# Performance work log

Hardware: AMD Instinct MI355X
Metric: run time of the kernel (lower is better)

## Reference

```python
import jax, jax.numpy as jnp
import numpy as np

TEMP = 0.5
LAMDA = 1.0
NUM_SLICE = 64
EPS = 1e-20


def _gaussian_kernel(size=11, sigma=1.5):
    coords = np.arange(size, dtype=np.float64) - (size - 1) / 2.0
    g = np.exp(-(coords ** 2) / (2.0 * sigma ** 2))
    g = g / g.sum()
    return jnp.asarray(g, dtype=jnp.float32)


def _ssim(x, y, data_range=1.0, win_size=11, sigma=1.5):
    # x, y: [B, S, H, W]; treat each slice as an independent 1-channel image.
    B, S, H, W = x.shape
    x4 = x.reshape(B * S, 1, H, W)
    y4 = y.reshape(B * S, 1, H, W)
    g = _gaussian_kernel(win_size, sigma)
    kh = g.reshape(1, 1, win_size, 1)
    kw = g.reshape(1, 1, 1, win_size)
    dn = ('NCHW', 'OIHW', 'NCHW')

    def blur(a):
        a = jax.lax.conv_general_dilated(a, kh, (1, 1), 'VALID', dimension_numbers=dn)
        a = jax.lax.conv_general_dilated(a, kw, (1, 1), 'VALID', dimension_numbers=dn)
        return a

    mu1 = blur(x4)
    mu2 = blur(y4)
    mu1_sq = mu1 * mu1
    mu2_sq = mu2 * mu2
    mu1_mu2 = mu1 * mu2
    sigma1_sq = blur(x4 * x4) - mu1_sq
    sigma2_sq = blur(y4 * y4) - mu2_sq
    sigma12 = blur(x4 * y4) - mu1_mu2
    C1 = (0.01 * data_range) ** 2
    C2 = (0.03 * data_range) ** 2
    ssim_map = ((2.0 * mu1_mu2 + C1) * (2.0 * sigma12 + C2)) / (
        (mu1_sq + mu2_sq + C1) * (sigma1_sq + sigma2_sq + C2))
    return jnp.mean(ssim_map)


def _l1(a, b):
    return jnp.mean(jnp.abs(a - b))


def _cumulative_mips(img_fake, target, gumbel, temp):
    # Growing-window gumbel-softmax MIP, computed in a single O(S) pass.
    # softmax over a prefix window is shift-invariant, so subtract the
    # per-pixel global max over the slice axis for stability, then use cumsums.
    y = img_fake + gumbel
    m = jnp.max(y, axis=1, keepdims=True)
    e = jnp.exp((y - m) / temp)                      # unnormalized softmax weights
    num = jnp.cumsum(e * img_fake, axis=1)
    den = jnp.cumsum(e, axis=1)
    pred_c1 = num / den                              # prefix windows [0:idx+1]
    target_c1 = jax.lax.cummax(target, axis=1)

    ef = jnp.flip(e, axis=1)
    xf = jnp.flip(img_fake, axis=1)
    num2 = jnp.cumsum(ef * xf, axis=1)
    den2 = jnp.cumsum(ef, axis=1)
    pred_c2 = num2 / den2                            # suffix windows [S-1-idx:]
    target_c2 = jax.lax.cummax(jnp.flip(target, axis=1), axis=1)
    return pred_c1, target_c1, pred_c2, target_c2


def _forward(img_fake, target, u_noise):
    gumbel = -jnp.log(-jnp.log(u_noise + EPS) + EPS)
    p1, t1, p2, t2 = _cumulative_mips(img_fake, target, gumbel, TEMP)
    loss_lissim = (_l1(img_fake, target) + 1.0 - _ssim(img_fake, target)) * LAMDA
    loss_mip_c1 = (_l1(p1, t1) + 1.0 - _ssim(p1, t1)) * LAMDA
    loss_mip_c2 = (_l1(p2, t2) + 1.0 - _ssim(p2, t2)) * LAMDA
    return loss_lissim + loss_mip_c1 + loss_mip_c2


def setup_inputs() -> dict:
    key = jax.random.key(0)
    k1, k2, k3 = jax.random.split(key, 3)
    shape = (2, NUM_SLICE, 256, 256)
    img_fake = jax.random.uniform(k1, shape, dtype=jnp.float32)
    target = jax.random.uniform(k2, shape, dtype=jnp.float32)
    u_noise = jax.random.uniform(k3, shape, dtype=jnp.float32)
    return {"img_fake": img_fake, "target": target, "u_noise": u_noise}


def reference(img_fake, target, u_noise):
    return _forward(img_fake, target, u_noise)
```

## Files before the change

### kernel.cpp

```cpp
#include <hip/hip_runtime.h>
#include <cmath>
#include <cstring>

#define NUM_S   64
#define IMG_H   256
#define IMG_W   256
#define HWSZ    (IMG_H*IMG_W)
#define BATCH   2
#define NPIX    (BATCH*HWSZ)
#define NEL     (BATCH*NUM_S*HWSZ)
#define NSLICE  (BATCH*NUM_S)
#define VALID   246
#define EPS_F   1e-20f
#define C1_F    1e-4f
#define C2_F    9e-4f
#define RS      264
#define FS      (16*RS)
#define NSLOT_SCAN 1024
#define NSLOT_ALL  7168
#define PTPAD   1024

typedef __fp16 half8  __attribute__((ext_vector_type(8)));
typedef __fp16 fp16x2 __attribute__((ext_vector_type(2)));
using fragC = __attribute__((ext_vector_type(4))) float;

union H8 { half8 v; short s[8]; int i[4]; };
union PK { fp16x2 v; int i; };
union HS { __fp16 f; short s; };

struct GH { short h[11]; };

__device__ inline fp16x2 pkrtz(float a, float b) {
    return __builtin_amdgcn_cvt_pkrtz(a, b);
}
__device__ inline float frcp(float x)  { return __builtin_amdgcn_rcpf(x); }
__device__ inline float flog2(float x) { return __builtin_amdgcn_logf(x); }
__device__ inline float fexp2(float x) { return __builtin_amdgcn_exp2f(x); }

__device__ inline void block_reduce_slot(float v, float* slot) {
    __shared__ float sm[8];
    __syncthreads();
    #pragma unroll
    for (int off = 32; off; off >>= 1) v += __shfl_down(v, off, 64);
    int lane = threadIdx.x & 63, w = threadIdx.x >> 6;
    if (lane == 0) sm[w] = v;
    __syncthreads();
    if (threadIdx.x == 0) {
        float s = 0.f;
        int nw = blockDim.x >> 6;
        for (int i = 0; i < nw; ++i) s += sm[i];
        *slot = s;
    }
}

__global__ __launch_bounds__(256) void scan_kernel(
    const float* __restrict__ img, const float* __restrict__ tgt,
    const float* __restrict__ un,
    uint2* __restrict__ pt0, uint2* __restrict__ pt1, uint2* __restrict__ pt2,
    float* __restrict__ slots)
{
    const int HW2 = HWSZ / 2;
    int tid = blockIdx.x * 256 + threadIdx.x;
    bool bwd = tid >= (NPIX / 2);
    int p2 = bwd ? tid - NPIX / 2 : tid;
    int b   = p2 >> 15;
    int hw2 = p2 & (HW2 - 1);
    int idx  = b * (NUM_S * HW2) + hw2 + (bwd ? (NUM_S - 1) * HW2 : 0);
    int step = bwd ? -HW2 : HW2;
    const float2* __restrict__ img2 = (const float2*)img;
    const float2* __restrict__ tgt2 = (const float2*)tgt;
    const float2* __restrict__ un2  = (const float2*)un;

    float num[2] = {0.f, 0.f}, den[2] = {0.f, 0.f}, tm[2] = {-INFINITY, -INFINITY};
    float l1x = 0.f, l1p = 0.f;

    float2 xb[4], ub[4], tb[4];
    #pragma unroll
    for (int j = 0; j < 4; ++j) {
        int id = idx + j * step;
        xb[j] = img2[id]; ub[j] = un2[id]; tb[j] = tgt2[id];
    }

    for (int i = 0; i < NUM_S; i += 4) {
        #pragma unroll
        for (int j = 0; j < 4; ++j) {
            float2 x = xb[j], u = ub[j], t = tb[j];
            if (i + j + 4 < NUM_S) {
                int id = idx + 4 * step;
                xb[j] = img2[id]; ub[j] = un2[id]; tb[j] = tgt2[id];
            }
            float xc[2] = {x.x, x.y}, uc[2] = {u.x, u.y}, tc[2] = {t.x, t.y};
            float p[2];
            #pragma unroll
            for (int c = 0; c < 2; ++c) {
                float w = fmaf(flog2(uc[c] + EPS_F), -0.6931471805599453f, EPS_F);
                float r = frcp(w);
                float e = fexp2(xc[c] * 2.8853900817779268f) * (r * r);
                num[c] = fmaf(e, xc[c], num[c]);
                den[c] += e;
                p[c] = num[c] * frcp(den[c]);
                tm[c] = fmaxf(tm[c], tc[c]);
                if (!bwd) l1x += fabsf(xc[c] - tc[c]);
                l1p += fabsf(p[c] - tm[c]);
            }
            PK k0, k1;
            k0.v = pkrtz(p[0], tm[0]); k1.v = pkrtz(p[1], tm[1]);
            uint2 pv = make_uint2((unsigned)k0.i, (unsigned)k1.i);
            if (!bwd) {
                PK a0, a1;
                a0.v = pkrtz(xc[0], tc[0]); a1.v = pkrtz(xc[1], tc[1]);
                pt0[idx] = make_uint2((unsigned)a0.i, (unsigned)a1.i);
                pt1[idx] = pv;
            } else {
                pt2[idx] = pv;
            }
            idx += step;
        }
    }
    block_reduce_slot(bwd ? 0.f : l1x, &slots[blockIdx.x]);
    block_reduce_slot(l1p, &slots[512 + blockIdx.x]);
}

__global__ __launch_bounds__(256) void ssim_kernel(
    const unsigned* __restrict__ pt0, const unsigned* __restrict__ pt1,
    const unsigned* __restrict__ pt2,
    GH gh, float* __restrict__ slots)
{
    __shared__ short Vl[5][FS];
    int pair  = blockIdx.z;
    int base  = blockIdx.y * HWSZ;
    int r0    = blockIdx.x * 16;
    int lane  = threadIdx.x & 63;
    int wid   = threadIdx.x >> 6;
    int q     = lane >> 4;
    int n     = lane & 15;

    H8 band;
    #pragma unroll
    for (int j = 0; j < 8; ++j) {
        int kk = q * 8 + j - n;
        short hv = 0;
        #pragma unroll
        for (int w = 0; w < 11; ++w) hv = (kk == w) ? gh.h[w] : hv;
        band.s[j] = hv;
    }

    for (int d = threadIdx.x; d < 320; d += 256) {
        int f = d >> 6, rm = d & 63, r = rm >> 2, cc = rm & 3;
        ((int*)Vl)[f * 2112 + r * 132 + 128 + cc] = 0;
    }

    const unsigned* __restrict__ pp =
        (pair == 0 ? pt0 : (pair == 1 ? pt1 : pt2)) + base;
    bool clampR = (r0 == 240);
    const fragC zero = {0.f, 0.f, 0.f, 0.f};

    unsigned ld[32];
    {
        int rowbase = r0 + q * 8;
        if (!clampR) {
            const unsigned* pb = pp + rowbase * IMG_W + n;
            #pragma unroll
            for (int it = 0; it < 4; ++it)
                #pragma unroll
                for (int j = 0; j < 8; ++j)
                    ld[it * 8 + j] = pb[j * IMG_W + (wid * 4 + it) * 16];
        } else {
            #pragma unroll
            for (int it = 0; it < 4; ++it)
                #pragma unroll
                for (int j = 0; j < 8; ++j) {
                    int rr = min(rowbase + j, IMG_H - 1);
                    ld[it * 8 + j] = pp[rr * IMG_W + (wid * 4 + it) * 16 + n];
                }
        }
    }
    #pragma unroll
    for (int it = 0; it < 4; ++it) {
        H8 fX, fY, fXX, fYY, fXY;
        #pragma unroll
        for (int j = 0; j < 4; ++j) {
            unsigned a = ld[it * 8 + 2 * j], b2 = ld[it * 8 + 2 * j + 1];
            fX.i[j] = (int)((a & 0xffffu) | (b2 << 16));
            fY.i[j] = (int)((a >> 16) | (b2 & 0xffff0000u));
        }
        fXX.v = fX.v * fX.v;
        fYY.v = fY.v * fY.v;
        fXY.v = fX.v * fY.v;
        fragC v0 = __builtin_amdgcn_mfma_f32_16x16x32_f16(band.v, fX.v,  zero, 0, 0, 0);
        fragC v1 = __builtin_amdgcn_mfma_f32_16x16x32_f16(band.v, fY.v,  zero, 0, 0, 0);
        fragC v2 = __builtin_amdgcn_mfma_f32_16x16x32_f16(band.v, fXX.v, zero, 0, 0, 0);
        fragC v3 = __builtin_amdgcn_mfma_f32_16x16x32_f16(band.v, fYY.v, zero, 0, 0, 0);
        fragC v4 = __builtin_amdgcn_mfma_f32_16x16x32_f16(band.v, fXY.v, zero, 0, 0, 0);
        int col = (wid * 4 + it) * 16 + n;
        #pragma unroll
        for (int reg = 0; reg < 4; ++reg) {
            int ro = (q * 4 + reg) * RS + col;
            HS cv;
            cv.f = (__fp16)v0[reg]; Vl[0][ro] = cv.s;
            cv.f = (__fp16)v1[reg]; Vl[1][ro] = cv.s;
            cv.f = (__fp16)v2[reg]; Vl[2][ro] = cv.s;
            cv.f = (__fp16)v3[reg]; Vl[3][ro] = cv.s;
            cv.f = (__fp16)v4[reg]; Vl[4][ro] = cv.s;
        }
    }
    __syncthreads();

    float lsum = 0.f;
    for (int it = 0; it < 4; ++it) {
        int c0 = (wid * 4 + it) * 16;
        int so = n * RS + c0 + q * 8;
        so = min(so, FS - 8);
        H8 a0, a1, a2, a3, a4;
        *(int4*)a0.i = *(const int4*)&Vl[0][so];
        *(int4*)a1.i = *(const int4*)&Vl[1][so];
        *(int4*)a2.i = *(const int4*)&Vl[2][so];
        *(int4*)a3.i = *(const int4*)&Vl[3][so];
        *(int4*)a4.i = *(const int4*)&Vl[4][so];
        fragC o0 = __builtin_amdgcn_mfma_f32_16x16x32_f16(a0.v, band.v, zero, 0, 0, 0);
        fragC o1 = __builtin_amdgcn_mfma_f32_16x16x32_f16(a1.v, band.v, zero, 0, 0, 0);
        fragC o2 = __builtin_amdgcn_mfma_f32_16x16x32_f16(a2.v, band.v, zero, 0, 0, 0);
        fragC o3 = __builtin_amdgcn_mfma_f32_16x16x32_f16(a3.v, band.v, zero, 0, 0, 0);
        fragC o4 = __builtin_amdgcn_mfma_f32_16x16x32_f16(a4.v, band.v, zero, 0, 0, 0);
        #pragma unroll
        for (int reg = 0; reg < 4; ++reg) {
            int r = r0 + q * 4 + reg;
            int c = c0 + n;
            if (r < VALID && c < VALID) {
                float m1 = o0[reg], m2 = o1[reg];
                float s11 = o2[reg] - m1 * m1;
                float s22 = o3[reg] - m2 * m2;
                float s12 = o4[reg] - m1 * m2;
                float nv = (2.f * m1 * m2 + C1_F) * (2.f * s12 + C2_F);
                float dv = (m1 * m1 + m2 * m2 + C1_F) * (s11 + s22 + C2_F);
                lsum += nv * frcp(dv);
            }
        }
    }
    block_reduce_slot(lsum,
        &slots[NSLOT_SCAN + pair * 2048 + blockIdx.y * 16 + blockIdx.x]);
}

__global__ void finalize_kernel(const float* __restrict__ slots,
                                float* __restrict__ out) {
    __shared__ double sa[4], sb[4];
    double a = 0.0, bsum = 0.0;
    for (int i = threadIdx.x; i < NSLOT_SCAN; i += 256) a += (double)slots[i];
    for (int i = NSLOT_SCAN + threadIdx.x; i < NSLOT_ALL; i += 256) bsum += (double)slots[i];
    #pragma unroll
    for (int off = 32; off; off >>= 1) {
        a    += __shfl_down(a, off, 64);
        bsum += __shfl_down(bsum, off, 64);
    }
    int lane = threadIdx.x & 63, w = threadIdx.x >> 6;
    if (lane == 0) { sa[w] = a; sb[w] = bsum; }
    __syncthreads();
    if (threadIdx.x == 0) {
        double A = sa[0] + sa[1] + sa[2] + sa[3];
        double B = sb[0] + sb[1] + sb[2] + sb[3];
        out[0] = (float)(3.0 + A / (double)NEL -
                         B / ((double)NSLICE * (double)VALID * (double)VALID));
    }
}

static unsigned short f32_to_f16(float f) {
    unsigned u; memcpy(&u, &f, 4);
    unsigned s = (u >> 16) & 0x8000u;
    int e = (int)((u >> 23) & 0xff) - 127 + 15;
    unsigned m = u & 0x7fffffu;
    unsigned h = s | ((unsigned)e << 10) | (m >> 13);
    unsigned rem = m & 0x1fffu;
    if (rem > 0x1000u || (rem == 0x1000u && (h & 1))) h++;
    return (unsigned short)h;
}
static double f16_to_d(unsigned short h) {
    unsigned e = (h >> 10) & 0x1f, m = h & 0x3ffu;
    return ldexp((double)(m + 1024), (int)e - 25);
}

extern "C" void kernel_launch(void* const* d_in, const int* in_sizes, int n_in,
                              void* d_out, int out_size, void* d_ws, size_t ws_size,
                              hipStream_t stream) {
    const float* img = (const float*)d_in[0];
    const float* tgt = (const float*)d_in[1];
    const float* un  = (const float*)d_in[2];
    float* out = (float*)d_out;

    unsigned* pt0 = (unsigned*)d_ws;
    unsigned* pt1 = pt0 + NEL + PTPAD;
    unsigned* pt2 = pt1 + NEL + PTPAD;
    float* slots = (float*)(pt2 + NEL);

    GH gh;
    {
        double g[11], s = 0.0;
        for (int i = 0; i < 11; ++i) { double d = i - 5; g[i] = exp(-d * d / 4.5); s += g[i]; }
        for (int i = 0; i < 11; ++i) g[i] /= s;
        for (int iter = 0; iter < 3; ++iter) {
            double sb = 0.0;
            unsigned short h[11];
            for (int i = 0; i < 11; ++i) { h[i] = f32_to_f16((float)g[i]); sb += f16_to_d(h[i]); }
            for (int i = 0; i < 11; ++i) { g[i] /= sb; gh.h[i] = (short)h[i]; }
        }
    }

    scan_kernel<<<NPIX / 256, 256, 0, stream>>>(img, tgt, un,
        (uint2*)pt0, (uint2*)pt1, (uint2*)pt2, slots);
    ssim_kernel<<<dim3(16, NSLICE, 3), 256, 0, stream>>>(pt0, pt1, pt2, gh, slots);
    finalize_kernel<<<1, 256, 0, stream>>>(slots, out);
}
```

Measured before the change: 202.8 us.

## Drop pt0 staging buffer; read raw inputs in SSIM pair 0 and scalarize scan

```diff
diff --git a/kernel.cpp b/kernel.cpp
--- a/kernel.cpp
+++ b/kernel.cpp
@@ -16,8 +16,8 @@
 #define C2_F    9e-4f
 #define RS      264
 #define FS      (16*RS)
-#define NSLOT_SCAN 1024
-#define NSLOT_ALL  7168
+#define NSLOT_SCAN 2048
+#define NSLOT_ALL  8192
 #define PTPAD   1024
 
 typedef __fp16 half8  __attribute__((ext_vector_type(8)));
@@ -56,74 +56,57 @@
 __global__ __launch_bounds__(256) void scan_kernel(
     const float* __restrict__ img, const float* __restrict__ tgt,
     const float* __restrict__ un,
-    uint2* __restrict__ pt0, uint2* __restrict__ pt1, uint2* __restrict__ pt2,
+    unsigned* __restrict__ pt1, unsigned* __restrict__ pt2,
     float* __restrict__ slots)
 {
-    const int HW2 = HWSZ / 2;
     int tid = blockIdx.x * 256 + threadIdx.x;
-    bool bwd = tid >= (NPIX / 2);
-    int p2 = bwd ? tid - NPIX / 2 : tid;
-    int b   = p2 >> 15;
-    int hw2 = p2 & (HW2 - 1);
-    int idx  = b * (NUM_S * HW2) + hw2 + (bwd ? (NUM_S - 1) * HW2 : 0);
-    int step = bwd ? -HW2 : HW2;
-    const float2* __restrict__ img2 = (const float2*)img;
-    const float2* __restrict__ tgt2 = (const float2*)tgt;
-    const float2* __restrict__ un2  = (const float2*)un;
-
-    float num[2] = {0.f, 0.f}, den[2] = {0.f, 0.f}, tm[2] = {-INFINITY, -INFINITY};
+    bool bwd = tid >= NPIX;
+    int p = bwd ? tid - NPIX : tid;
+    int b  = p >> 16;
+    int hw = p & (HWSZ - 1);
+    int idx  = b * (NUM_S * HWSZ) + hw + (bwd ? (NUM_S - 1) * HWSZ : 0);
+    int step = bwd ? -HWSZ : HWSZ;
+    unsigned* __restrict__ pt = bwd ? pt2 : pt1;
+
+    float num = 0.f, den = 0.f, tm = -INFINITY;
     float l1x = 0.f, l1p = 0.f;
 
-    float2 xb[4], ub[4], tb[4];
+    float xb[4], ub[4], tb[4];
     #pragma unroll
     for (int j = 0; j < 4; ++j) {
         int id = idx + j * step;
-        xb[j] = img2[id]; ub[j] = un2[id]; tb[j] = tgt2[id];
+        xb[j] = img[id]; ub[j] = un[id]; tb[j] = tgt[id];
     }
 
     for (int i = 0; i < NUM_S; i += 4) {
         #pragma unroll
         for (int j = 0; j < 4; ++j) {
-            float2 x = xb[j], u = ub[j], t = tb[j];
+            float x = xb[j], u = ub[j], t = tb[j];
             if (i + j + 4 < NUM_S) {
                 int id = idx + 4 * step;
-                xb[j] = img2[id]; ub[j] = un2[id]; tb[j] = tgt2[id];
+                xb[j] = img[id]; ub[j] = un[id]; tb[j] = tgt[id];
             }
-            float xc[2] = {x.x, x.y}, uc[2] = {u.x, u.y}, tc[2] = {t.x, t.y};
-            float p[2];
-            #pragma unroll
-            for (int c = 0; c < 2; ++c) {
-                float w = fmaf(flog2(uc[c] + EPS_F), -0.6931471805599453f, EPS_F);
-                float r = frcp(w);
-                float e = fexp2(xc[c] * 2.8853900817779268f) * (r * r);
-                num[c] = fmaf(e, xc[c], num[c]);
-                den[c] += e;
-                p[c] = num[c] * frcp(den[c]);
-                tm[c] = fmaxf(tm[c], tc[c]);
-                if (!bwd) l1x += fabsf(xc[c] - tc[c]);
-                l1p += fabsf(p[c] - tm[c]);
-            }
-            PK k0, k1;
-            k0.v = pkrtz(p[0], tm[0]); k1.v = pkrtz(p[1], tm[1]);
-            uint2 pv = make_uint2((unsigned)k0.i, (unsigned)k1.i);
-            if (!bwd) {
-                PK a0, a1;
-                a0.v = pkrtz(xc[0], tc[0]); a1.v = pkrtz(xc[1], tc[1]);
-                pt0[idx] = make_uint2((unsigned)a0.i, (unsigned)a1.i);
-                pt1[idx] = pv;
-            } else {
-                pt2[idx] = pv;
-            }
+            float w = fmaf(flog2(u + EPS_F), -0.6931471805599453f, EPS_F);
+            float r = frcp(w);
+            float e = fexp2(x * 2.8853900817779268f) * (r * r);
+            num = fmaf(e, x, num);
+            den += e;
+            float pv = num * frcp(den);
+            tm = fmaxf(tm, t);
+            if (!bwd) l1x += fabsf(x - t);
+            l1p += fabsf(pv - tm);
+            PK k; k.v = pkrtz(pv, tm);
+            pt[idx] = (unsigned)k.i;
             idx += step;
         }
     }
     block_reduce_slot(bwd ? 0.f : l1x, &slots[blockIdx.x]);
-    block_reduce_slot(l1p, &slots[512 + blockIdx.x]);
+    block_reduce_slot(l1p, &slots[1024 + blockIdx.x]);
 }
 
 __global__ __launch_bounds__(256) void ssim_kernel(
-    const unsigned* __restrict__ pt0, const unsigned* __restrict__ pt1,
-    const unsigned* __restrict__ pt2,
+    const float* __restrict__ img, const float* __restrict__ tgt,
+    const unsigned* __restrict__ pt1, const unsigned* __restrict__ pt2,
     GH gh, float* __restrict__ slots)
 {
     __shared__ short Vl[5][FS];
@@ -150,29 +133,55 @@
         ((int*)Vl)[f * 2112 + r * 132 + 128 + cc] = 0;
     }
 
-    const unsigned* __restrict__ pp =
-        (pair == 0 ? pt0 : (pair == 1 ? pt1 : pt2)) + base;
     bool clampR = (r0 == 240);
     const fragC zero = {0.f, 0.f, 0.f, 0.f};
 
     unsigned ld[32];
     {
         int rowbase = r0 + q * 8;
-        if (!clampR) {
-            const unsigned* pb = pp + rowbase * IMG_W + n;
-            #pragma unroll
-            for (int it = 0; it < 4; ++it)
+        if (pair == 0) {
+            const float* ia = img + base;
+            const float* ib = tgt + base;
+            if (!clampR) {
+                const float* pa = ia + rowbase * IMG_W + n;
+                const float* pb = ib + rowbase * IMG_W + n;
                 #pragma unroll
-                for (int j = 0; j < 8; ++j)
-                    ld[it * 8 + j] = pb[j * IMG_W + (wid * 4 + it) * 16];
+                for (int it = 0; it < 4; ++it)
+                    #pragma unroll
+                    for (int j = 0; j < 8; ++j) {
+                        int o = j * IMG_W + (wid * 4 + it) * 16;
+                        PK k; k.v = pkrtz(pa[o], pb[o]);
+                        ld[it * 8 + j] = (unsigned)k.i;
+                    }
+            } else {
+                #pragma unroll
+                for (int it = 0; it < 4; ++it)
+                    #pragma unroll
+                    for (int j = 0; j < 8; ++j) {
+                        int rr = min(rowbase + j, IMG_H - 1);
+                        int o = rr * IMG_W + (wid * 4 + it) * 16 + n;
+                        PK k; k.v = pkrtz(ia[o], ib[o]);
+                        ld[it * 8 + j] = (unsigned)k.i;
+                    }
+            }
         } else {
-            #pragma unroll
-            for (int it = 0; it < 4; ++it)
+            const unsigned* __restrict__ pp = (pair == 1 ? pt1 : pt2) + base;
+            if (!clampR) {
+                const unsigned* pb = pp + rowbase * IMG_W + n;
                 #pragma unroll
-                for (int j = 0; j < 8; ++j) {
-                    int rr = min(rowbase + j, IMG_H - 1);
-                    ld[it * 8 + j] = pp[rr * IMG_W + (wid * 4 + it) * 16 + n];
-                }
+                for (int it = 0; it < 4; ++it)
+                    #pragma unroll
+                    for (int j = 0; j < 8; ++j)
+                        ld[it * 8 + j] = pb[j * IMG_W + (wid * 4 + it) * 16];
+            } else {
+                #pragma unroll
+                for (int it = 0; it < 4; ++it)
+                    #pragma unroll
+                    for (int j = 0; j < 8; ++j) {
+                        int rr = min(rowbase + j, IMG_H - 1);
+                        ld[it * 8 + j] = pp[rr * IMG_W + (wid * 4 + it) * 16 + n];
+                    }
+            }
         }
     }
     #pragma unroll
@@ -286,8 +295,7 @@
     const float* un  = (const float*)d_in[2];
     float* out = (float*)d_out;
 
-    unsigned* pt0 = (unsigned*)d_ws;
-    unsigned* pt1 = pt0 + NEL + PTPAD;
+    unsigned* pt1 = (unsigned*)d_ws;
     unsigned* pt2 = pt1 + NEL + PTPAD;
     float* slots = (float*)(pt2 + NEL);
 
@@ -304,8 +312,7 @@
         }
     }
 
-    scan_kernel<<<NPIX / 256, 256, 0, stream>>>(img, tgt, un,
-        (uint2*)pt0, (uint2*)pt1, (uint2*)pt2, slots);
-    ssim_kernel<<<dim3(16, NSLICE, 3), 256, 0, stream>>>(pt0, pt1, pt2, gh, slots);
+    scan_kernel<<<2 * NPIX / 256, 256, 0, stream>>>(img, tgt, un, pt1, pt2, slots);
+    ssim_kernel<<<dim3(16, NSLICE, 3), 256, 0, stream>>>(img, tgt, pt1, pt2, gh, slots);
     finalize_kernel<<<1, 256, 0, stream>>>(slots, out);
 }
```

After: 216.2 us. 6.6% more time.

## Swizzle SSIM LDS tile layout, deepen scan prefetch, reuse LDS for reduction

Applied to the files above, without the earlier changes.

```diff
diff --git a/kernel.cpp b/kernel.cpp
--- a/kernel.cpp
+++ b/kernel.cpp
@@ -14,8 +14,7 @@
 #define EPS_F   1e-20f
 #define C1_F    1e-4f
 #define C2_F    9e-4f
-#define RS      264
-#define FS      (16*RS)
+#define FSH     4096
 #define NSLOT_SCAN 1024
 #define NSLOT_ALL  7168
 #define PTPAD   1024
@@ -49,6 +48,19 @@
         float s = 0.f;
         int nw = blockDim.x >> 6;
         for (int i = 0; i < nw; ++i) s += sm[i];
+        *slot = s;
+    }
+}
+
+__device__ inline void block_reduce_vl(float v, float* slot, float* sm) {
+    __syncthreads();
+    #pragma unroll
+    for (int off = 32; off; off >>= 1) v += __shfl_down(v, off, 64);
+    int lane = threadIdx.x & 63, w = threadIdx.x >> 6;
+    if (lane == 0) sm[w] = v;
+    __syncthreads();
+    if (threadIdx.x == 0) {
+        float s = sm[0] + sm[1] + sm[2] + sm[3];
         *slot = s;
     }
 }
@@ -74,19 +86,19 @@
     float num[2] = {0.f, 0.f}, den[2] = {0.f, 0.f}, tm[2] = {-INFINITY, -INFINITY};
     float l1x = 0.f, l1p = 0.f;
 
-    float2 xb[4], ub[4], tb[4];
-    #pragma unroll
-    for (int j = 0; j < 4; ++j) {
+    float2 xb[8], ub[8], tb[8];
+    #pragma unroll
+    for (int j = 0; j < 8; ++j) {
         int id = idx + j * step;
         xb[j] = img2[id]; ub[j] = un2[id]; tb[j] = tgt2[id];
     }
 
-    for (int i = 0; i < NUM_S; i += 4) {
-        #pragma unroll
-        for (int j = 0; j < 4; ++j) {
+    for (int i = 0; i < NUM_S; i += 8) {
+        #pragma unroll
+        for (int j = 0; j < 8; ++j) {
             float2 x = xb[j], u = ub[j], t = tb[j];
-            if (i + j + 4 < NUM_S) {
-                int id = idx + 4 * step;
+            if (i + j + 8 < NUM_S) {
+                int id = idx + 8 * step;
                 xb[j] = img2[id]; ub[j] = un2[id]; tb[j] = tgt2[id];
             }
             float xc[2] = {x.x, x.y}, uc[2] = {u.x, u.y}, tc[2] = {t.x, t.y};
@@ -126,7 +138,7 @@
     const unsigned* __restrict__ pt2,
     GH gh, float* __restrict__ slots)
 {
-    __shared__ short Vl[5][FS];
+    __shared__ short Vl[5][FSH];
     int pair  = blockIdx.z;
     int base  = blockIdx.y * HWSZ;
     int r0    = blockIdx.x * 16;
@@ -143,11 +155,6 @@
         #pragma unroll
         for (int w = 0; w < 11; ++w) hv = (kk == w) ? gh.h[w] : hv;
         band.s[j] = hv;
-    }
-
-    for (int d = threadIdx.x; d < 320; d += 256) {
-        int f = d >> 6, rm = d & 63, r = rm >> 2, cc = rm & 3;
-        ((int*)Vl)[f * 2112 + r * 132 + 128 + cc] = 0;
     }
 
     const unsigned* __restrict__ pp =
@@ -195,7 +202,8 @@
         int col = (wid * 4 + it) * 16 + n;
         #pragma unroll
         for (int reg = 0; reg < 4; ++reg) {
-            int ro = (q * 4 + reg) * RS + col;
+            int r = q * 4 + reg;
+            int ro = (r << 8) + (col ^ ((r & 7) << 3));
             HS cv;
             cv.f = (__fp16)v0[reg]; Vl[0][ro] = cv.s;
             cv.f = (__fp16)v1[reg]; Vl[1][ro] = cv.s;
@@ -209,8 +217,9 @@
     float lsum = 0.f;
     for (int it = 0; it < 4; ++it) {
         int c0 = (wid * 4 + it) * 16;
-        int so = n * RS + c0 + q * 8;
-        so = min(so, FS - 8);
+        int cb = c0 + q * 8;
+        if (cb > 248) cb = 248;
+        int so = (n << 8) + (cb ^ ((n & 7) << 3));
         H8 a0, a1, a2, a3, a4;
         *(int4*)a0.i = *(const int4*)&Vl[0][so];
         *(int4*)a1.i = *(const int4*)&Vl[1][so];
@@ -237,8 +246,9 @@
             }
         }
     }
-    block_reduce_slot(lsum,
-        &slots[NSLOT_SCAN + pair * 2048 + blockIdx.y * 16 + blockIdx.x]);
+    block_reduce_vl(lsum,
+        &slots[NSLOT_SCAN + pair * 2048 + blockIdx.y * 16 + blockIdx.x],
+        (float*)Vl);
 }
 
 __global__ void finalize_kernel(const float* __restrict__ slots,
```

After: 195.7 us. 1.04x faster.
